# Kernel tuning notes

Hardware: AMD Instinct MI355X
Metric: run time of the kernel (lower is better)

## Reference

```python
import jax, jax.numpy as jnp
import numpy as np

N = 50000      # nodes
E = 800000     # edges (before self loops)
NF = 4         # node feature dim
EF = 4         # edge feature dim
EMB = 16       # joint embedding dim
HID = 64       # hidden dim
OUT = 128      # output dim
H = 4          # heads (layers 0,1); last layer has 1 head
NEG_SLOPE = 0.2


def setup_inputs() -> dict:
    key = jax.random.key(0)
    ks = jax.random.split(key, 20)
    in0 = NF + EMB  # 20

    def lin(k, o, i):
        return (jax.random.normal(k, (o, i), jnp.float32) * np.float32(1.0 / np.sqrt(i)))

    return {
        'x': jax.random.normal(ks[0], (N, NF), jnp.float32),
        'edge_index': jax.random.randint(ks[1], (2, E), 0, N, dtype=jnp.int32),
        'edge_attr': jax.random.normal(ks[2], (E, EF), jnp.float32),
        'joint_types': jax.random.randint(ks[3], (N,), 0, 17, dtype=jnp.int32),
        'emb_table': jax.random.normal(ks[4], (17, EMB), jnp.float32) * 0.1,
        'W0': lin(ks[5], H * HID, in0),
        'a_src0': jax.random.normal(ks[6], (H, HID), jnp.float32) * 0.1,
        'a_dst0': jax.random.normal(ks[7], (H, HID), jnp.float32) * 0.1,
        'We0': lin(ks[8], H, EF),
        'W1': lin(ks[9], H * HID, HID),
        'a_src1': jax.random.normal(ks[10], (H, HID), jnp.float32) * 0.1,
        'a_dst1': jax.random.normal(ks[11], (H, HID), jnp.float32) * 0.1,
        'We1': lin(ks[12], H, EF),
        'W2': lin(ks[13], 1 * OUT, HID),
        'a_src2': jax.random.normal(ks[14], (1, OUT), jnp.float32) * 0.1,
        'a_dst2': jax.random.normal(ks[15], (1, OUT), jnp.float32) * 0.1,
        'We2': lin(ks[16], 1, EF),
    }


def gat_layer(x, src, dst, eattr, W, a_src, a_dst, We, num_nodes):
    # x: [N, F_in]; W: [H*C, F_in]; a_src/a_dst: [H, C]; We: [H, EF]
    Hh, C = a_src.shape
    h = (x @ W.T).reshape(num_nodes, Hh, C)  # [N, H, C]
    # per-node attention scores, gathered per edge (same math as per-edge dot)
    s_i = jnp.einsum('nhc,hc->nh', h, a_src)  # applied to x_i = x[dst]
    s_j = jnp.einsum('nhc,hc->nh', h, a_dst)  # applied to x_j = x[src]
    alpha = s_i[dst] + s_j[src] + eattr @ We.T  # [Etot, H]
    alpha = jax.nn.leaky_relu(alpha, NEG_SLOPE)
    # faithful to torch.softmax(alpha, dim=0): GLOBAL softmax over all edges per head
    alpha = jax.nn.softmax(alpha, axis=0)
    msgs = h[src] * alpha[:, :, None]  # [Etot, H, C]
    out = jax.ops.segment_sum(msgs, dst, num_segments=num_nodes)  # aggr='add'
    return out.mean(axis=1)  # update(): mean over heads -> [N, C]


def reference(x, edge_index, edge_attr, joint_types, emb_table,
              W0, a_src0, a_dst0, We0,
              W1, a_src1, a_dst1, We1,
              W2, a_src2, a_dst2, We2):
    num_nodes = x.shape[0]
    # add self loops (edge_attr fill 0.0)
    loops = jnp.arange(num_nodes, dtype=edge_index.dtype)
    src = jnp.concatenate([edge_index[0], loops])
    dst = jnp.concatenate([edge_index[1], loops])
    eattr = jnp.concatenate([edge_attr, jnp.zeros((num_nodes, edge_attr.shape[1]), edge_attr.dtype)], axis=0)

    h = jnp.concatenate([x, emb_table[joint_types]], axis=-1)  # [N, 20]
    h = gat_layer(h, src, dst, eattr, W0, a_src0, a_dst0, We0, num_nodes)
    h = jax.nn.elu(h)  # dropout is identity in eval mode
    h = gat_layer(h, src, dst, eattr, W1, a_src1, a_dst1, We1, num_nodes)
    h = jax.nn.elu(h)
    h = gat_layer(h, src, dst, eattr, W2, a_src2, a_dst2, We2, num_nodes)
    return h  # [N, OUT]
```

## Files before the change

### kernel.cpp

```cpp
#include <hip/hip_runtime.h>
#include <math.h>

#define NN 50000
#define EE 800000
#define EEN (EE+NN)
#define STRIDE 64
#define NFEAT 4
#define EFEAT 4
#define EMBD 16
#define IN0 20
#define HIDD 64
#define OUTD 128
#define EDGE_NB 1024

__device__ __forceinline__ unsigned short f2bf(float f){
  unsigned u = __float_as_uint(f);
  return (unsigned short)((u + 0x7FFFu + ((u>>16)&1u)) >> 16);
}
__device__ __forceinline__ float bfl(unsigned u){ return __uint_as_float(u<<16); }
__device__ __forceinline__ float bfh(unsigned u){ return __uint_as_float(u & 0xFFFF0000u); }

template<int V> struct ldt;
template<> struct ldt<4>{ using T = uint2; };
template<> struct ldt<2>{ using T = unsigned int; };

__global__ void k_init(int* fill){
  int i = blockIdx.x*blockDim.x + threadIdx.x;
  if (i < NN) fill[i]=0;
}

__global__ void k_scatter(const int* __restrict__ ei, const float4* __restrict__ eattr,
                          int* fill, int* __restrict__ col, float4* __restrict__ eacsr){
  int idx = blockIdx.x*blockDim.x + threadIdx.x;
  if (idx < EE){
    int d = ei[EE+idx];
    int pos = atomicAdd(&fill[d],1);
    int slot = d*STRIDE + 1 + pos;
    col[slot] = ei[idx];
    eacsr[slot] = eattr[idx];
  } else if (idx < EEN){
    int n = idx-EE;
    col[n*STRIDE] = n;
  }
}

template<int F_IN,int HH,int CC>
__device__ __forceinline__ void av_one(const float* W, const float* asrc,
                                       const float* adst, float* av, int tid){
  if (tid >= HH*F_IN) return;
  int h = tid / F_IN, f = tid % F_IN;
  float s1=0.f, s2=0.f;
  for (int c=0;c<CC;c++){
    float wv = W[(size_t)(h*CC+c)*F_IN+f];
    s1 += asrc[h*CC+c]*wv;
    s2 += adst[h*CC+c]*wv;
  }
  av[tid] = s1;
  av[HH*F_IN+tid] = s2;
}
__global__ void k_av3(const float* W0, const float* as0, const float* ad0, float* av0,
                      const float* W1, const float* as1, const float* ad1, float* av1,
                      const float* W2, const float* as2, const float* ad2, float* av2,
                      float* zred){
  int tid = threadIdx.x;
  if      (blockIdx.x==0){ av_one<IN0,4,64> (W0, as0, ad0, av0, tid); if (tid<192) zred[tid]=0.f; }
  else if (blockIdx.x==1) av_one<64,4,64>  (W1, as1, ad1, av1, tid);
  else                    av_one<64,1,128> (W2, as2, ad2, av2, tid);
}

template<int K,int NCOL,int HH,bool CONCAT>
__global__ __launch_bounds__(256)
void k_gemm(const float* __restrict__ xin, const int* __restrict__ jt,
            const float* __restrict__ emb, const float* __restrict__ W,
            const float* __restrict__ avp, unsigned short* __restrict__ hout,
            float* __restrict__ si, float* __restrict__ sj){
  constexpr int PITCH = 132;
  __shared__ float xT[K*PITCH];
  __shared__ float wT[K*PITCH];
  __shared__ float EMBL[CONCAT ? 17*EMBD : 1];
  int tid = threadIdx.x;
  int rbase = blockIdx.x*128, cbase = blockIdx.y*128;
  if (CONCAT){
    for (int i=tid; i<17*EMBD; i+=256) EMBL[i]=emb[i];
    __syncthreads();
    if (tid < 128){
      int row = tid;
      int gr = rbase+row; if (gr >= NN) gr = NN-1;
      float4 v = ((const float4*)xin)[gr];
      xT[0*PITCH+row]=v.x; xT[1*PITCH+row]=v.y;
      xT[2*PITCH+row]=v.z; xT[3*PITCH+row]=v.w;
      int j = jt[gr];
      #pragma unroll
      for (int k=0;k<EMBD;k++) xT[(NFEAT+k)*PITCH+row] = EMBL[j*EMBD+k];
    } else {
      int col = tid-128;
      const float4* wp = (const float4*)(W + (size_t)(cbase+col)*K);
      #pragma unroll
      for (int k4=0;k4<K/4;k4++){
        float4 v = wp[k4];
        wT[(4*k4+0)*PITCH+col]=v.x; wT[(4*k4+1)*PITCH+col]=v.y;
        wT[(4*k4+2)*PITCH+col]=v.z; wT[(4*k4+3)*PITCH+col]=v.w;
      }
    }
  } else {
    constexpr int K4 = K/4;
    for (int i=tid; i<128*K4; i+=256){
      int row = i/K4, k4 = i%K4;
      int gr = rbase+row; if (gr >= NN) gr = NN-1;
      float4 v = ((const float4*)xin)[(size_t)gr*K4 + k4];
      xT[(4*k4+0)*PITCH+row]=v.x; xT[(4*k4+1)*PITCH+row]=v.y;
      xT[(4*k4+2)*PITCH+row]=v.z; xT[(4*k4+3)*PITCH+row]=v.w;
    }
    for (int i=tid; i<128*K4; i+=256){
      int col = i/K4, k4 = i%K4;
      float4 v = ((const float4*)W)[(size_t)(cbase+col)*K4 + k4];
      wT[(4*k4+0)*PITCH+col]=v.x; wT[(4*k4+1)*PITCH+col]=v.y;
      wT[(4*k4+2)*PITCH+col]=v.z; wT[(4*k4+3)*PITCH+col]=v.w;
    }
  }
  __syncthreads();
  int lane = tid & 63, w = tid >> 6;
  int r0 = (w>>1)*64 + (lane&7)*8;
  int c0 = (w&1)*64 + (lane>>3)*8;
  float acc[8][8];
  #pragma unroll
  for (int i=0;i<8;i++)
    #pragma unroll
    for (int j=0;j<8;j++) acc[i][j]=0.f;
  #pragma unroll 4
  for (int k=0;k<K;k++){
    float a[8], b[8];
    *(float4*)&a[0] = *(const float4*)&xT[k*PITCH + r0];
    *(float4*)&a[4] = *(const float4*)&xT[k*PITCH + r0 + 4];
    *(float4*)&b[0] = *(const float4*)&wT[k*PITCH + c0];
    *(float4*)&b[4] = *(const float4*)&wT[k*PITCH + c0 + 4];
    #pragma unroll
    for (int i=0;i<8;i++)
      #pragma unroll
      for (int j=0;j<8;j++) acc[i][j] += a[i]*b[j];
  }
  if (blockIdx.y==0 && tid < 128){
    int row = tid, gr = rbase+row;
    if (gr < NN){
      #pragma unroll
      for (int h=0;h<HH;h++){
        float a=0.f, b=0.f;
        for (int k=0;k<K;k++){
          float xv = xT[k*PITCH+row];
          a += xv*avp[h*K+k];
          b += xv*avp[HH*K+h*K+k];
        }
        si[(size_t)gr*HH+h]=a;
        sj[(size_t)gr*HH+h]=b;
      }
    }
  }
  #pragma unroll
  for (int i=0;i<8;i++){
    int n = rbase + r0 + i;
    if (n < NN){
      uint4 o;
      o.x = (unsigned)f2bf(acc[i][0]) | ((unsigned)f2bf(acc[i][1])<<16);
      o.y = (unsigned)f2bf(acc[i][2]) | ((unsigned)f2bf(acc[i][3])<<16);
      o.z = (unsigned)f2bf(acc[i][4]) | ((unsigned)f2bf(acc[i][5])<<16);
      o.w = (unsigned)f2bf(acc[i][6]) | ((unsigned)f2bf(acc[i][7])<<16);
      *(uint4*)(hout + (size_t)n*NCOL + cbase + c0) = o;
    }
  }
}

template<int HH>
__global__ __launch_bounds__(256)
void k_edge2(const int* __restrict__ col, const float4* __restrict__ eacsr,
             const int* __restrict__ fill, const float* __restrict__ We,
             const float* __restrict__ si, const float* __restrict__ sj,
             float* __restrict__ pp, float* __restrict__ zred){
  int wave = threadIdx.x>>6, lane = threadIdx.x&63;
  float z[HH];
  #pragma unroll
  for (int h=0;h<HH;h++) z[h]=0.f;
  for (int n = blockIdx.x*4 + wave; n < NN; n += EDGE_NB*4){
    int cnt = 1 + fill[n];
    if (lane < cnt){
      int slot = n*STRIDE + lane;
      int s = col[slot];
      float4 ea;
      if (lane==0){ ea = make_float4(0.f,0.f,0.f,0.f); }
      else        { ea = eacsr[slot]; }
      if (HH==4){
        float4 siv = ((const float4*)si)[n];
        float4 sjv = ((const float4*)sj)[s];
        float te[4] = {siv.x+sjv.x, siv.y+sjv.y, siv.z+sjv.z, siv.w+sjv.w};
        float pv[4];
        #pragma unroll
        for (int h=0;h<4;h++){
          float t = te[h] + ea.x*We[h*EFEAT+0] + ea.y*We[h*EFEAT+1]
                          + ea.z*We[h*EFEAT+2] + ea.w*We[h*EFEAT+3];
          t = (t>0.f)? t : 0.2f*t;
          float p = expf(t);
          z[h]+=p; pv[h]=p;
        }
        ((float4*)pp)[slot] = make_float4(pv[0],pv[1],pv[2],pv[3]);
      } else {
        float t = si[n] + sj[s]
                + ea.x*We[0] + ea.y*We[1] + ea.z*We[2] + ea.w*We[3];
        t = (t>0.f)? t : 0.2f*t;
        float p = expf(t);
        z[0]+=p;
        pp[slot] = p;
      }
    }
  }
  __shared__ float zs[4][HH];
  #pragma unroll
  for (int h=0;h<HH;h++){
    float v=z[h];
    #pragma unroll
    for (int off=32; off>0; off>>=1) v += __shfl_xor(v,off,64);
    if (lane==0) zs[wave][h]=v;
  }
  __syncthreads();
  if (threadIdx.x < HH){
    float tot = zs[0][threadIdx.x]+zs[1][threadIdx.x]
              + zs[2][threadIdx.x]+zs[3][threadIdx.x];
    atomicAdd(&zred[threadIdx.x*16], tot);
  }
}

template<int HH,int CC,bool DO_ELU>
__global__ __launch_bounds__(256)
void k_agg(const unsigned short* __restrict__ hb, const float* __restrict__ pp,
           const float* __restrict__ zred, const int* __restrict__ fill,
           const int* __restrict__ col, float* __restrict__ outp){
  constexpr int HC = HH*CC;
  constexpr int V  = HC/64;
  using LT = typename ldt<V>::T;
  int wave = threadIdx.x>>6, lane = threadIdx.x&63;
  int n = blockIdx.x*4 + wave;
  int hd = (lane*V)/CC;
  float invZ = 1.0f/zred[hd*16];
  float acc[V];
  #pragma unroll
  for (int v=0;v<V;v++) acc[v]=0.f;
  auto mac = [&](float p, LT h){
    if constexpr (V==4){
      acc[0] += p*bfl(h.x); acc[1] += p*bfh(h.x);
      acc[2] += p*bfl(h.y); acc[3] += p*bfh(h.y);
    } else {
      acc[0] += p*bfl(h);   acc[1] += p*bfh(h);
    }
  };
  int beg = n*STRIDE, end = beg + 1 + fill[n];
  int i = beg;
  for (; i+8<=end; i+=8){
    int sr[8]; float p[8]; LT h[8];
    #pragma unroll
    for (int k=0;k<8;k++) sr[k]=col[i+k];
    #pragma unroll
    for (int k=0;k<8;k++)
      p[k] = (HH==4) ? pp[(size_t)(i+k)*4+hd] : pp[i+k];
    #pragma unroll
    for (int k=0;k<8;k++) h[k]=((const LT*)(hb + (size_t)sr[k]*HC))[lane];
    #pragma unroll
    for (int k=0;k<8;k++) mac(p[k], h[k]);
  }
  for (; i<end; i++){
    int sr = col[i];
    float p = (HH==4) ? pp[(size_t)i*4+hd] : pp[i];
    LT h = ((const LT*)(hb + (size_t)sr*HC))[lane];
    mac(p, h);
  }
  #pragma unroll
  for (int v=0;v<V;v++) acc[v] *= invZ;
  if (HH==4){
    #pragma unroll
    for (int off=16; off<64; off<<=1){
      #pragma unroll
      for (int v=0;v<V;v++) acc[v] += __shfl_xor(acc[v], off, 64);
    }
    if (lane < 16){
      float4 o;
      o.x=0.25f*acc[0]; o.y=0.25f*acc[1]; o.z=0.25f*acc[2]; o.w=0.25f*acc[3];
      if (DO_ELU){
        o.x = (o.x>0.f)? o.x : expm1f(o.x);
        o.y = (o.y>0.f)? o.y : expm1f(o.y);
        o.z = (o.z>0.f)? o.z : expm1f(o.z);
        o.w = (o.w>0.f)? o.w : expm1f(o.w);
      }
      ((float4*)outp)[(size_t)n*(CC/4)+lane] = o;
    }
  } else {
    float2 o; o.x=acc[0]; o.y=acc[1];
    if (DO_ELU){
      o.x = (o.x>0.f)? o.x : expm1f(o.x);
      o.y = (o.y>0.f)? o.y : expm1f(o.y);
    }
    ((float2*)outp)[(size_t)n*(CC/2)+lane] = o;
  }
}

extern "C" void kernel_launch(void* const* d_in, const int* in_sizes, int n_in,
                              void* d_out, int out_size, void* d_ws, size_t ws_size,
                              hipStream_t stream){
  const float* x    = (const float*)d_in[0];
  const int*   ei   = (const int*)d_in[1];
  const float* eatt = (const float*)d_in[2];
  const int*   jt   = (const int*)d_in[3];
  const float* emb  = (const float*)d_in[4];
  const float* W0   = (const float*)d_in[5];
  const float* as0  = (const float*)d_in[6];
  const float* ad0  = (const float*)d_in[7];
  const float* We0  = (const float*)d_in[8];
  const float* W1   = (const float*)d_in[9];
  const float* as1  = (const float*)d_in[10];
  const float* ad1  = (const float*)d_in[11];
  const float* We1  = (const float*)d_in[12];
  const float* W2   = (const float*)d_in[13];
  const float* as2  = (const float*)d_in[14];
  const float* ad2  = (const float*)d_in[15];
  const float* We2  = (const float*)d_in[16];
  float* out = (float*)d_out;

  char* p = (char*)d_ws;
  auto alloc = [&](size_t bytes)->char*{
    char* r = p; p += (bytes + 255) & ~(size_t)255; return r;
  };
  unsigned short* hbuf = (unsigned short*)alloc((size_t)NN*256*2);
  float* x1     = (float*)alloc((size_t)NN*64*4);
  float* x2     = (float*)alloc((size_t)NN*64*4);
  float* si     = (float*)alloc((size_t)NN*4*4);
  float* sj     = (float*)alloc((size_t)NN*4*4);
  float* pp     = (float*)alloc((size_t)NN*STRIDE*16);
  int*   fill   = (int*)alloc((size_t)NN*4);
  int*   col    = (int*)alloc((size_t)NN*STRIDE*4);
  float4* eacsr = (float4*)alloc((size_t)NN*STRIDE*16);
  float* av0    = (float*)alloc(512*4);
  float* av1    = (float*)alloc(512*4);
  float* av2    = (float*)alloc(512*4);
  float* zred   = (float*)alloc(192*4);

  k_init   <<<dim3((NN+255)/256),  256, 0, stream>>>(fill);
  k_scatter<<<dim3((EEN+255)/256), 256, 0, stream>>>(ei, (const float4*)eatt,
                                                     fill, col, eacsr);
  k_av3    <<<dim3(3),             256, 0, stream>>>(W0,as0,ad0,av0, W1,as1,ad1,av1,
                                                     W2,as2,ad2,av2, zred);

  dim3 gg01((NN+127)/128, 2);
  dim3 gg2 ((NN+127)/128, 1);
  dim3 egrid2(EDGE_NB);
  dim3 ngrid(NN/4);

  k_gemm<IN0,256,4,true> <<<gg01, 256, 0, stream>>>(x, jt, emb, W0, av0, hbuf, si, sj);
  k_edge2<4>             <<<egrid2,256, 0, stream>>>(col, eacsr, fill, We0, si, sj, pp, zred+0);
  k_agg<4,64,true>       <<<ngrid,256, 0, stream>>>(hbuf, pp, zred+0, fill, col, x1);

  k_gemm<64,256,4,false> <<<gg01, 256, 0, stream>>>(x1, jt, emb, W1, av1, hbuf, si, sj);
  k_edge2<4>             <<<egrid2,256, 0, stream>>>(col, eacsr, fill, We1, si, sj, pp, zred+64);
  k_agg<4,64,true>       <<<ngrid,256, 0, stream>>>(hbuf, pp, zred+64, fill, col, x2);

  k_gemm<64,128,1,false> <<<gg2,  256, 0, stream>>>(x2, jt, emb, W2, av2, hbuf, si, sj);
  k_edge2<1>             <<<egrid2,256, 0, stream>>>(col, eacsr, fill, We2, si, sj, pp, zred+128);
  k_agg<1,128,false>     <<<ngrid,256, 0, stream>>>(hbuf, pp, zred+128, fill, col, out);
}
```

Before: 495.5 us.

## Pack edge records into 16-byte structs with fp16 attrs and probabilities

Merges the separate column-index and edge-attribute CSR arrays into one 16-byte record per slot, storing edge attributes as fp16. The edge kernel writes fp16 per-head probabilities together with the source index, so the aggregation kernel reads one record instead of separate col and pp arrays. Both kernels use nontemporal loads on these streams. The aim is fewer memory transactions and bytes in the edge and aggregate passes, at the cost of fp16 rounding of edge attributes and attention weights. fp16 weights could overflow if exp(t) exceeds the fp16 range.

Result: slower. 523.2 us (+5.6%).

```diff
diff --git a/kernel.cpp b/kernel.cpp
--- a/kernel.cpp
+++ b/kernel.cpp
@@ -20,6 +20,22 @@
 __device__ __forceinline__ float bfl(unsigned u){ return __uint_as_float(u<<16); }
 __device__ __forceinline__ float bfh(unsigned u){ return __uint_as_float(u & 0xFFFF0000u); }
 
+__device__ __forceinline__ unsigned f2h2(float a, float b){
+  _Float16 ha=(_Float16)a, hb=(_Float16)b;
+  unsigned short ua=*(unsigned short*)&ha, ub=*(unsigned short*)&hb;
+  return (unsigned)ua | ((unsigned)ub<<16);
+}
+__device__ __forceinline__ float h2f(unsigned short u){
+  _Float16 h=*(_Float16*)&u; return (float)h;
+}
+
+typedef unsigned uv4 __attribute__((ext_vector_type(4)));
+typedef unsigned uv2 __attribute__((ext_vector_type(2)));
+template<typename T>
+__device__ __forceinline__ T ntload(const T* p){
+  return __builtin_nontemporal_load(const_cast<T*>(p));
+}
+
 template<int V> struct ldt;
 template<> struct ldt<4>{ using T = uint2; };
 template<> struct ldt<2>{ using T = unsigned int; };
@@ -30,17 +46,20 @@
 }
 
 __global__ void k_scatter(const int* __restrict__ ei, const float4* __restrict__ eattr,
-                          int* fill, int* __restrict__ col, float4* __restrict__ eacsr){
+                          int* fill, uv4* __restrict__ erec){
   int idx = blockIdx.x*blockDim.x + threadIdx.x;
   if (idx < EE){
     int d = ei[EE+idx];
+    int s = ei[idx];
+    float4 ea = eattr[idx];
     int pos = atomicAdd(&fill[d],1);
     int slot = d*STRIDE + 1 + pos;
-    col[slot] = ei[idx];
-    eacsr[slot] = eattr[idx];
+    uv4 r; r.x=(unsigned)s; r.y=f2h2(ea.x,ea.y); r.z=f2h2(ea.z,ea.w); r.w=0u;
+    erec[slot]=r;
   } else if (idx < EEN){
     int n = idx-EE;
-    col[n*STRIDE] = n;
+    uv4 r; r.x=(unsigned)n; r.y=0u; r.z=0u; r.w=0u;
+    erec[n*STRIDE]=r;
   }
 }
 
@@ -171,10 +190,10 @@
 
 template<int HH>
 __global__ __launch_bounds__(256)
-void k_edge2(const int* __restrict__ col, const float4* __restrict__ eacsr,
-             const int* __restrict__ fill, const float* __restrict__ We,
-             const float* __restrict__ si, const float* __restrict__ sj,
-             float* __restrict__ pp, float* __restrict__ zred){
+void k_edge2(const uv4* __restrict__ erec, const int* __restrict__ fill,
+             const float* __restrict__ We, const float* __restrict__ si,
+             const float* __restrict__ sj, unsigned* __restrict__ prec,
+             float* __restrict__ zred){
   int wave = threadIdx.x>>6, lane = threadIdx.x&63;
   float z[HH];
   #pragma unroll
@@ -183,10 +202,10 @@
     int cnt = 1 + fill[n];
     if (lane < cnt){
       int slot = n*STRIDE + lane;
-      int s = col[slot];
-      float4 ea;
-      if (lane==0){ ea = make_float4(0.f,0.f,0.f,0.f); }
-      else        { ea = eacsr[slot]; }
+      uv4 r = ntload(&erec[slot]);
+      int s = (int)r.x;
+      float eax=h2f((unsigned short)(r.y&0xFFFFu)), eay=h2f((unsigned short)(r.y>>16));
+      float eaz=h2f((unsigned short)(r.z&0xFFFFu)), eaw=h2f((unsigned short)(r.z>>16));
       if (HH==4){
         float4 siv = ((const float4*)si)[n];
         float4 sjv = ((const float4*)sj)[s];
@@ -194,20 +213,22 @@
         float pv[4];
         #pragma unroll
         for (int h=0;h<4;h++){
-          float t = te[h] + ea.x*We[h*EFEAT+0] + ea.y*We[h*EFEAT+1]
-                          + ea.z*We[h*EFEAT+2] + ea.w*We[h*EFEAT+3];
+          float t = te[h] + eax*We[h*EFEAT+0] + eay*We[h*EFEAT+1]
+                          + eaz*We[h*EFEAT+2] + eaw*We[h*EFEAT+3];
           t = (t>0.f)? t : 0.2f*t;
           float p = expf(t);
           z[h]+=p; pv[h]=p;
         }
-        ((float4*)pp)[slot] = make_float4(pv[0],pv[1],pv[2],pv[3]);
+        uv4 o; o.x=f2h2(pv[0],pv[1]); o.y=f2h2(pv[2],pv[3]); o.z=(unsigned)s; o.w=0u;
+        ((uv4*)prec)[slot] = o;
       } else {
         float t = si[n] + sj[s]
-                + ea.x*We[0] + ea.y*We[1] + ea.z*We[2] + ea.w*We[3];
+                + eax*We[0] + eay*We[1] + eaz*We[2] + eaw*We[3];
         t = (t>0.f)? t : 0.2f*t;
         float p = expf(t);
         z[0]+=p;
-        pp[slot] = p;
+        uv2 o; o.x=__float_as_uint(p); o.y=(unsigned)s;
+        ((uv2*)prec)[slot] = o;
       }
     }
   }
@@ -229,15 +250,16 @@
 
 template<int HH,int CC,bool DO_ELU>
 __global__ __launch_bounds__(256)
-void k_agg(const unsigned short* __restrict__ hb, const float* __restrict__ pp,
+void k_agg(const unsigned short* __restrict__ hb, const unsigned* __restrict__ prec,
            const float* __restrict__ zred, const int* __restrict__ fill,
-           const int* __restrict__ col, float* __restrict__ outp){
+           float* __restrict__ outp){
   constexpr int HC = HH*CC;
   constexpr int V  = HC/64;
   using LT = typename ldt<V>::T;
   int wave = threadIdx.x>>6, lane = threadIdx.x&63;
   int n = blockIdx.x*4 + wave;
   int hd = (lane*V)/CC;
+  int hw = hd>>1, hs = (hd&1)*16;
   float invZ = 1.0f/zred[hd*16];
   float acc[V];
   #pragma unroll
@@ -255,18 +277,35 @@
   for (; i+8<=end; i+=8){
     int sr[8]; float p[8]; LT h[8];
     #pragma unroll
-    for (int k=0;k<8;k++) sr[k]=col[i+k];
-    #pragma unroll
-    for (int k=0;k<8;k++)
-      p[k] = (HH==4) ? pp[(size_t)(i+k)*4+hd] : pp[i+k];
+    for (int k=0;k<8;k++){
+      if (HH==4){
+        uv4 q = ntload(&((const uv4*)prec)[i+k]);
+        sr[k] = (int)q.z;
+        unsigned wd = hw ? q.y : q.x;
+        p[k] = h2f((unsigned short)(wd>>hs));
+      } else {
+        uv2 q = ntload(&((const uv2*)prec)[i+k]);
+        p[k] = __uint_as_float(q.x);
+        sr[k] = (int)q.y;
+      }
+    }
     #pragma unroll
     for (int k=0;k<8;k++) h[k]=((const LT*)(hb + (size_t)sr[k]*HC))[lane];
     #pragma unroll
     for (int k=0;k<8;k++) mac(p[k], h[k]);
   }
   for (; i<end; i++){
-    int sr = col[i];
-    float p = (HH==4) ? pp[(size_t)i*4+hd] : pp[i];
+    int sr; float p;
+    if (HH==4){
+      uv4 q = ntload(&((const uv4*)prec)[i]);
+      sr = (int)q.z;
+      unsigned wd = hw ? q.y : q.x;
+      p = h2f((unsigned short)(wd>>hs));
+    } else {
+      uv2 q = ntload(&((const uv2*)prec)[i]);
+      p = __uint_as_float(q.x);
+      sr = (int)q.y;
+    }
     LT h = ((const LT*)(hb + (size_t)sr*HC))[lane];
     mac(p, h);
   }
@@ -330,10 +369,9 @@
   float* x2     = (float*)alloc((size_t)NN*64*4);
   float* si     = (float*)alloc((size_t)NN*4*4);
   float* sj     = (float*)alloc((size_t)NN*4*4);
-  float* pp     = (float*)alloc((size_t)NN*STRIDE*16);
+  unsigned* prec= (unsigned*)alloc((size_t)NN*STRIDE*16);
   int*   fill   = (int*)alloc((size_t)NN*4);
-  int*   col    = (int*)alloc((size_t)NN*STRIDE*4);
-  float4* eacsr = (float4*)alloc((size_t)NN*STRIDE*16);
+  uv4*   erec   = (uv4*)alloc((size_t)NN*STRIDE*16);
   float* av0    = (float*)alloc(512*4);
   float* av1    = (float*)alloc(512*4);
   float* av2    = (float*)alloc(512*4);
@@ -341,7 +379,7 @@
 
   k_init   <<<dim3((NN+255)/256),  256, 0, stream>>>(fill);
   k_scatter<<<dim3((EEN+255)/256), 256, 0, stream>>>(ei, (const float4*)eatt,
-                                                     fill, col, eacsr);
+                                                     fill, erec);
   k_av3    <<<dim3(3),             256, 0, stream>>>(W0,as0,ad0,av0, W1,as1,ad1,av1,
                                                      W2,as2,ad2,av2, zred);
 
@@ -351,14 +389,14 @@
   dim3 ngrid(NN/4);
 
   k_gemm<IN0,256,4,true> <<<gg01, 256, 0, stream>>>(x, jt, emb, W0, av0, hbuf, si, sj);
-  k_edge2<4>             <<<egrid2,256, 0, stream>>>(col, eacsr, fill, We0, si, sj, pp, zred+0);
-  k_agg<4,64,true>       <<<ngrid,256, 0, stream>>>(hbuf, pp, zred+0, fill, col, x1);
+  k_edge2<4>             <<<egrid2,256, 0, stream>>>(erec, fill, We0, si, sj, prec, zred+0);
+  k_agg<4,64,true>       <<<ngrid,256, 0, stream>>>(hbuf, prec, zred+0, fill, x1);
 
   k_gemm<64,256,4,false> <<<gg01, 256, 0, stream>>>(x1, jt, emb, W1, av1, hbuf, si, sj);
-  k_edge2<4>             <<<egrid2,256, 0, stream>>>(col, eacsr, fill, We1, si, sj, pp, zred+64);
-  k_agg<4,64,true>       <<<ngrid,256, 0, stream>>>(hbuf, pp, zred+64, fill, col, x2);
+  k_edge2<4>             <<<egrid2,256, 0, stream>>>(erec, fill, We1, si, sj, prec, zred+64);
+  k_agg<4,64,true>       <<<ngrid,256, 0, stream>>>(hbuf, prec, zred+64, fill, x2);
 
   k_gemm<64,128,1,false> <<<gg2,  256, 0, stream>>>(x2, jt, emb, W2, av2, hbuf, si, sj);
-  k_edge2<1>             <<<egrid2,256, 0, stream>>>(col, eacsr, fill, We2, si, sj, pp, zred+128);
-  k_agg<1,128,false>     <<<ngrid,256, 0, stream>>>(hbuf, pp, zred+128, fill, col, out);
-}
+  k_edge2<1>             <<<egrid2,256, 0, stream>>>(erec, fill, We2, si, sj, prec, zred+128);
+  k_agg<1,128,false>     <<<ngrid,256, 0, stream>>>(hbuf, prec, zred+128, fill, out);
+}
```
